# Kernel tuning notes

Measured on AMD Instinct MI355X. Metric: run time of the kernel, lower is better.

The kernel has to match this reference:

```python
import jax, jax.numpy as jnp
import numpy as np

B = 2048      # graphs per side
NPG = 40      # nodes per graph
N = B * NPG   # 81920 total nodes
E = 4 * N     # 327680 directed edges
IN_DIM = 74
H = 256
ADD = 8
GCR_LAYERS = 5
MLP1, MLP2 = 1024, 512


def setup_inputs() -> dict:
    key = jax.random.key(0)
    ks = jax.random.split(key, 24)
    n2g = jnp.repeat(jnp.arange(B, dtype=jnp.int32), NPG)
    s = 0.05
    d = {
        'cat_src': jax.random.randint(ks[0], (E,), 0, N, dtype=jnp.int32),
        'cat_dst': jax.random.randint(ks[1], (E,), 0, N, dtype=jnp.int32),
        'cat_n2g': n2g,
        'cat_x': jax.random.normal(ks[2], (N, IN_DIM), jnp.float32),
        'an_src': jax.random.randint(ks[3], (E,), 0, N, dtype=jnp.int32),
        'an_dst': jax.random.randint(ks[4], (E,), 0, N, dtype=jnp.int32),
        'an_n2g': n2g,
        'an_x': jax.random.normal(ks[5], (N, IN_DIM), jnp.float32),
        'add_features': jax.random.normal(ks[6], (B, ADD), jnp.float32),
        # shared GNN params (same module processes cation and anion)
        'W0': jax.random.normal(ks[7], (IN_DIM, H), jnp.float32) * s,
        'b0': jnp.zeros((H,), jnp.float32),
        'gcrW': jax.random.normal(ks[8], (GCR_LAYERS, 2, H, H), jnp.float32) * s,
        'gcrb': jnp.zeros((GCR_LAYERS, 2, H), jnp.float32),
        # MLP head: (2H + ADD) -> 1024 -> 512 -> 1
        'mW1': jax.random.normal(ks[9], (2 * H + ADD, MLP1), jnp.float32) * s,
        'mb1': jnp.zeros((MLP1,), jnp.float32),
        'mW2': jax.random.normal(ks[10], (MLP1, MLP2), jnp.float32) * s,
        'mb2': jnp.zeros((MLP2,), jnp.float32),
        'mW3': jax.random.normal(ks[11], (MLP2, 1), jnp.float32) * s,
        'mb3': jnp.zeros((1,), jnp.float32),
    }
    return d


def _graph_conv(src, dst, x, W, b):
    # DGL GraphConv, norm='both': out = D_in^{-1/2} A^T D_out^{-1/2} x W + b
    ones = jnp.ones(src.shape[0], x.dtype)
    deg_out = jnp.clip(jax.ops.segment_sum(ones, src, num_segments=N), 1.0)
    deg_in = jnp.clip(jax.ops.segment_sum(ones, dst, num_segments=N), 1.0)
    h = x * jax.lax.rsqrt(deg_out)[:, None]
    agg = jax.ops.segment_sum(h[src], dst, num_segments=N)  # [N, d]
    return (agg * jax.lax.rsqrt(deg_in)[:, None]) @ W + b


def _feat_extract(src, dst, n2g, x, W0, b0, gcrW, gcrb):
    h = _graph_conv(src, dst, x, W0, b0)  # no activation after first conv
    for i in range(GCR_LAYERS):
        o1 = _graph_conv(src, dst, h, gcrW[i, 0], gcrb[i, 0])
        o2 = _graph_conv(src, dst, jax.nn.relu(o1), gcrW[i, 1], gcrb[i, 1])
        h = jax.nn.relu(o2)  # res_connection = 0 -> plain replace
    # dgl.sum_nodes readout per graph
    return jax.ops.segment_sum(h, n2g, num_segments=B)  # [B, H]


def _leaky(x):
    return jnp.where(x > 0, x, 0.01 * x)  # nn.LeakyReLU default slope


def reference(cat_src, cat_dst, cat_n2g, cat_x, an_src, an_dst, an_n2g, an_x,
              add_features, W0, b0, gcrW, gcrb, mW1, mb1, mW2, mb2, mW3, mb3):
    cat_feat = _feat_extract(cat_src, cat_dst, cat_n2g, cat_x, W0, b0, gcrW, gcrb)
    an_feat = _feat_extract(an_src, an_dst, an_n2g, an_x, W0, b0, gcrW, gcrb)
    z = jnp.concatenate([cat_feat, an_feat, add_features], axis=1)  # [B, 2H+ADD]
    h = _leaky(z @ mW1 + mb1)
    h = _leaky(h @ mW2 + mb2)
    out = h @ mW3 + mb3  # [B, 1]
    return out.squeeze(-1)
```

## Files before the change

### kernel.cpp

```cpp
#include <hip/hip_runtime.h>


#define NN 81920
#define NN2 163840
#define NE 327680
#define NE2 655360
#define NB 2048
#define NB2 4096
#define H 256
#define INDIM 74
#define KPAD 128
#define ZK 576
#define DEGCAP 32
#define BSTAGE 24
#define TM 64
#define CPITCH 132

typedef unsigned short u16;
typedef __attribute__((ext_vector_type(8))) short short8;
typedef __attribute__((ext_vector_type(4))) float f32x4;

__device__ inline u16 f2b(float f) {
    unsigned u = __builtin_bit_cast(unsigned, f);
    u += 0x7fffu + ((u >> 16) & 1u);
    return (u16)(u >> 16);
}
__device__ inline float b2f(u16 b) {
    unsigned u = ((unsigned)b) << 16;
    return __builtin_bit_cast(float, u);
}
__device__ inline float blo(unsigned u) { return __builtin_bit_cast(float, u << 16); }
__device__ inline float bhi(unsigned u) { return __builtin_bit_cast(float, u & 0xffff0000u); }

__global__ void fill_kernel(const int* __restrict__ cs, const int* __restrict__ cd,
                            const int* __restrict__ as_, const int* __restrict__ ad,
                            int* __restrict__ dego, int* __restrict__ cnti,
                            int* __restrict__ bucket) {
    int e = blockIdx.x * 256 + threadIdx.x;
    if (e < NE2) {
        int s, d;
        if (e < NE) { s = cs[e]; d = cd[e]; }
        else        { s = as_[e - NE] + NN; d = ad[e - NE] + NN; }
        atomicAdd(&dego[s], 1);
        int p = atomicAdd(&cnti[d], 1);
        if (p < DEGCAP) bucket[(size_t)p * NN2 + d] = s;
    }
}

__global__ void rsqrt_kernel(const int* __restrict__ dego, const int* __restrict__ cnti,
                             float* __restrict__ rso, float* __restrict__ rsi) {
    int i = blockIdx.x * 256 + threadIdx.x;
    if (i < NN2) {
        rso[i] = rsqrtf((float)(dego[i] > 1 ? dego[i] : 1));
        rsi[i] = rsqrtf((float)(cnti[i] > 1 ? cnti[i] : 1));
    }
}

__global__ __launch_bounds__(256) void prescale_x_kernel(
        const float* __restrict__ cx, const float* __restrict__ ax,
        const float* __restrict__ rso, u16* __restrict__ xbp) {
    int t = threadIdx.x;
    int node = blockIdx.x * 4 + (t >> 6);
    int lane = t & 63;
    const float* x = (node < NN) ? (cx + (size_t)node * INDIM)
                                 : (ax + (size_t)(node - NN) * INDIM);
    float w = rso[node];
    int f0 = lane * 2, f1 = f0 + 1;
    u16 a = (f0 < INDIM) ? f2b(x[f0] * w) : (u16)0;
    u16 b = (f1 < INDIM) ? f2b(x[f1] * w) : (u16)0;
    ((unsigned*)xbp)[(size_t)node * 64 + lane] = a | ((unsigned)b << 16);
}

__global__ void prep_w0_kernel(const float* __restrict__ W0, u16* __restrict__ Wt0) {
    int i = blockIdx.x * 256 + threadIdx.x;
    int n = i >> 7, k = i & 127;
    float v = (k < INDIM) ? W0[(size_t)k * H + n] : 0.f;
    Wt0[i] = f2b(v);
}

__global__ void prep_gcr_kernel(const float* __restrict__ W, u16* __restrict__ Wt) {
    int i = blockIdx.x * 256 + threadIdx.x;
    int l = blockIdx.y;
    int n = i >> 8, k = i & 255;
    Wt[(size_t)l * 65536 + i] = f2b(W[(size_t)l * 65536 + (size_t)k * H + n]);
}

__global__ void prep_w1_kernel(const float* __restrict__ W, u16* __restrict__ Wt) {
    int i = blockIdx.x * 256 + threadIdx.x;
    if (i >= 1024 * ZK) return;
    int n = i / ZK, k = i - n * ZK;
    float v = (k < 520) ? W[(size_t)k * 1024 + n] : 0.f;
    Wt[i] = f2b(v);
}

__global__ void prep_w2_kernel(const float* __restrict__ W, u16* __restrict__ Wt) {
    int i = blockIdx.x * 256 + threadIdx.x;
    int n = i >> 10, k = i & 1023;
    Wt[i] = f2b(W[(size_t)k * 512 + n]);
}

__device__ inline void ldg_lds16(const u16* g, u16* l) {
    __builtin_amdgcn_global_load_lds(
        (const __attribute__((address_space(1))) unsigned int*)g,
        (__attribute__((address_space(3))) unsigned int*)l, 16, 0, 0);
}
__device__ inline float actf(float v, int act) {
    if (act == 1) return fmaxf(v, 0.f);
    if (act == 2) return (v > 0.f) ? v : 0.01f * v;
    return v;
}

template <int KD, bool RSO>
__global__ __launch_bounds__(512, 6) void fused_conv_kernel(
        const u16* __restrict__ hIn, const int* __restrict__ bucket,
        const int* __restrict__ cnti, const float* __restrict__ rso,
        const float* __restrict__ rsi, const u16* __restrict__ Bt,
        const float* __restrict__ bias, u16* __restrict__ hOut,
        int act) {
    constexpr int NCH = KD / 8;
    constexpr int KT  = KD / 64;
    __shared__ __align__(16) u16 smem[TM * KD + 8192];
    u16* As = smem;
    u16* Bs = smem + TM * KD;
    int* bkLds = (int*)Bs;
    int* cntL  = (int*)Bs + BSTAGE * TM;

    int t = threadIdx.x;
    int n0 = blockIdx.x * TM;

#pragma unroll
    for (int i = 0; i < (BSTAGE * TM) / 512; ++i) {
        int idx = i * 512 + t;
        bkLds[idx] = bucket[(size_t)(idx >> 6) * NN2 + n0 + (idx & 63)];
    }
    if (t < TM) cntL[t] = cnti[n0 + t];
    __syncthreads();

    for (int i = 0; i < (TM * NCH) / 512; ++i) {
        int gid = i * 512 + t;
        int nl = gid / NCH;
        int ch = gid - nl * NCH;
        int node = n0 + nl;
        int deg = cntL[nl]; if (deg > DEGCAP) deg = DEGCAP;
        int degL = deg < BSTAGE ? deg : BSTAGE;
        const int* bkcol = bkLds + nl;
        int fc = ch * 8;
        int s0 = (deg > 0) ? bkcol[0] : node;
        int sx[8];
#pragma unroll
        for (int s = 0; s < 8; ++s) {
            int raw = bkcol[s * TM];
            sx[s] = (s < degL) ? raw : s0;
        }
        uint4 vx[8];
#pragma unroll
        for (int s = 0; s < 8; ++s)
            vx[s] = *(const uint4*)(hIn + (size_t)sx[s] * KD + fc);
        float wx[8];
#pragma unroll
        for (int s = 0; s < 8; ++s) {
            float rw = RSO ? rso[sx[s]] : 1.f;
            wx[s] = (s < degL) ? rw : 0.f;
        }
        float acc[8] = {};
#pragma unroll
        for (int s = 0; s < 8; ++s) {
            acc[0] += blo(vx[s].x) * wx[s];
            acc[1] += bhi(vx[s].x) * wx[s];
            acc[2] += blo(vx[s].y) * wx[s];
            acc[3] += bhi(vx[s].y) * wx[s];
            acc[4] += blo(vx[s].z) * wx[s];
            acc[5] += bhi(vx[s].z) * wx[s];
            acc[6] += blo(vx[s].w) * wx[s];
            acc[7] += bhi(vx[s].w) * wx[s];
        }
        for (int base = 8; base < degL; base += 4) {
            int i0 = bkcol[(base + 0) * TM];
            int i1 = (base + 1 < degL) ? bkcol[(base + 1) * TM] : i0;
            int i2 = (base + 2 < degL) ? bkcol[(base + 2) * TM] : i0;
            int i3 = (base + 3 < degL) ? bkcol[(base + 3) * TM] : i0;
            float w0 = (RSO ? rso[i0] : 1.f);
            float w1 = (base + 1 < degL) ? (RSO ? rso[i1] : 1.f) : 0.f;
            float w2 = (base + 2 < degL) ? (RSO ? rso[i2] : 1.f) : 0.f;
            float w3 = (base + 3 < degL) ? (RSO ? rso[i3] : 1.f) : 0.f;
            uint4 v0 = *(const uint4*)(hIn + (size_t)i0 * KD + fc);
            uint4 v1 = *(const uint4*)(hIn + (size_t)i1 * KD + fc);
            uint4 v2 = *(const uint4*)(hIn + (size_t)i2 * KD + fc);
            uint4 v3 = *(const uint4*)(hIn + (size_t)i3 * KD + fc);
            acc[0] += blo(v0.x) * w0 + blo(v1.x) * w1 + blo(v2.x) * w2 + blo(v3.x) * w3;
            acc[1] += bhi(v0.x) * w0 + bhi(v1.x) * w1 + bhi(v2.x) * w2 + bhi(v3.x) * w3;
            acc[2] += blo(v0.y) * w0 + blo(v1.y) * w1 + blo(v2.y) * w2 + blo(v3.y) * w3;
            acc[3] += bhi(v0.y) * w0 + bhi(v1.y) * w1 + bhi(v2.y) * w2 + bhi(v3.y) * w3;
            acc[4] += blo(v0.z) * w0 + blo(v1.z) * w1 + blo(v2.z) * w2 + blo(v3.z) * w3;
            acc[5] += bhi(v0.z) * w0 + bhi(v1.z) * w1 + bhi(v2.z) * w2 + bhi(v3.z) * w3;
            acc[6] += blo(v0.w) * w0 + blo(v1.w) * w1 + blo(v2.w) * w2 + blo(v3.w) * w3;
            acc[7] += bhi(v0.w) * w0 + bhi(v1.w) * w1 + bhi(v2.w) * w2 + bhi(v3.w) * w3;
        }
        if (deg > BSTAGE) {
            for (int base = BSTAGE; base < deg; base += 4) {
                int i0 = bucket[(size_t)(base + 0) * NN2 + node];
                int i1 = (base + 1 < deg) ? bucket[(size_t)(base + 1) * NN2 + node] : i0;
                int i2 = (base + 2 < deg) ? bucket[(size_t)(base + 2) * NN2 + node] : i0;
                int i3 = (base + 3 < deg) ? bucket[(size_t)(base + 3) * NN2 + node] : i0;
                float w0 = (RSO ? rso[i0] : 1.f);
                float w1 = (base + 1 < deg) ? (RSO ? rso[i1] : 1.f) : 0.f;
                float w2 = (base + 2 < deg) ? (RSO ? rso[i2] : 1.f) : 0.f;
                float w3 = (base + 3 < deg) ? (RSO ? rso[i3] : 1.f) : 0.f;
                uint4 v0 = *(const uint4*)(hIn + (size_t)i0 * KD + fc);
                uint4 v1 = *(const uint4*)(hIn + (size_t)i1 * KD + fc);
                uint4 v2 = *(const uint4*)(hIn + (size_t)i2 * KD + fc);
                uint4 v3 = *(const uint4*)(hIn + (size_t)i3 * KD + fc);
                acc[0] += blo(v0.x) * w0 + blo(v1.x) * w1 + blo(v2.x) * w2 + blo(v3.x) * w3;
                acc[1] += bhi(v0.x) * w0 + bhi(v1.x) * w1 + bhi(v2.x) * w2 + bhi(v3.x) * w3;
                acc[2] += blo(v0.y) * w0 + blo(v1.y) * w1 + blo(v2.y) * w2 + blo(v3.y) * w3;
                acc[3] += bhi(v0.y) * w0 + bhi(v1.y) * w1 + bhi(v2.y) * w2 + bhi(v3.y) * w3;
                acc[4] += blo(v0.z) * w0 + blo(v1.z) * w1 + blo(v2.z) * w2 + blo(v3.z) * w3;
                acc[5] += bhi(v0.z) * w0 + bhi(v1.z) * w1 + bhi(v2.z) * w2 + bhi(v3.z) * w3;
                acc[6] += blo(v0.w) * w0 + blo(v1.w) * w1 + blo(v2.w) * w2 + blo(v3.w) * w3;
                acc[7] += bhi(v0.w) * w0 + bhi(v1.w) * w1 + bhi(v2.w) * w2 + bhi(v3.w) * w3;
            }
        }
        float ri = rsi[node];
        u16 o[8];
#pragma unroll
        for (int j = 0; j < 8; ++j) o[j] = f2b(acc[j] * ri);
        uint4 ov;
        ov.x = o[0] | ((unsigned)o[1] << 16);
        ov.y = o[2] | ((unsigned)o[3] << 16);
        ov.z = o[4] | ((unsigned)o[5] << 16);
        ov.w = o[6] | ((unsigned)o[7] << 16);
        int kt = ch >> 3, seg = ch & 7;
        *(uint4*)(As + (size_t)kt * (TM * 64) + nl * 64 + ((seg ^ (nl & 7)) * 8)) = ov;
    }
    __syncthreads();

    int wave = t >> 6, lane = t & 63;
    int wr = wave >> 2, wc = wave & 3;
    int mrow = lane & 15, q = lane >> 4;

    f32x4 acc[2][4] = {};
    for (int kt = 0; kt < KT; ++kt) {
        const u16* Ak = As + kt * (TM * 64);
#pragma unroll
        for (int nh = 0; nh < 2; ++nh) {
#pragma unroll
            for (int c = 0; c < 2; ++c) {
                int cidx = c * 512 + t;
                int row = cidx >> 3, seg = cidx & 7;
                int ks = ((seg ^ (row & 7))) * 8;
                ldg_lds16(Bt + (size_t)(nh * 128 + row) * KD + kt * 64 + ks,
                          Bs + (size_t)(c * 512 + wave * 64) * 8);
            }
            __syncthreads();
#pragma unroll
            for (int kk = 0; kk < 2; ++kk) {
                short8 a[2], b[2];
#pragma unroll
                for (int mt = 0; mt < 2; ++mt) {
                    int row = wr * 32 + mt * 16 + mrow;
                    int seg = (kk * 4 + q) ^ (row & 7);
                    a[mt] = *(const short8*)(Ak + row * 64 + seg * 8);
                }
#pragma unroll
                for (int nt = 0; nt < 2; ++nt) {
                    int row = wc * 32 + nt * 16 + mrow;
                    int seg = (kk * 4 + q) ^ (row & 7);
                    b[nt] = *(const short8*)(Bs + row * 64 + seg * 8);
                }
#pragma unroll
                for (int mt = 0; mt < 2; ++mt)
#pragma unroll
                    for (int nt = 0; nt < 2; ++nt)
                        acc[mt][nh * 2 + nt] = __builtin_amdgcn_mfma_f32_16x16x32_bf16(
                            a[mt], b[nt], acc[mt][nh * 2 + nt], 0, 0, 0);
            }
            __syncthreads();
        }
    }

#pragma unroll
    for (int nh = 0; nh < 2; ++nh) {
#pragma unroll
        for (int mt = 0; mt < 2; ++mt) {
            int rl = wr * 32 + mt * 16 + q * 4;
#pragma unroll
            for (int nt = 0; nt < 2; ++nt) {
                int cl = wc * 32 + nt * 16 + mrow;
                float bv = bias[nh * 128 + cl];
#pragma unroll
                for (int qq = 0; qq < 4; ++qq) {
                    float v = actf(acc[mt][nh * 2 + nt][qq] + bv, act);
                    smem[(size_t)(rl + qq) * CPITCH + cl] = f2b(v);
                }
            }
        }
        __syncthreads();
        int rr = t >> 4, sg = t & 15;
#pragma unroll
        for (int pass = 0; pass < 2; ++pass) {
            int row = pass * 32 + rr;
            uint4 val = *(const uint4*)(smem + (size_t)row * CPITCH + sg * 8);
            *(uint4*)(hOut + (size_t)(n0 + row) * 256 + nh * 128 + sg * 8) = val;
        }
        __syncthreads();
    }
}

__global__ __launch_bounds__(256) void gemm_mfma_kernel(
        const u16* __restrict__ A, int lda,
        const u16* __restrict__ Bt, int ldb,
        const float* __restrict__ bias, u16* __restrict__ C, int ldc,
        int Kiters, int act) {
    __shared__ __align__(16) u16 smem[128 * CPITCH];
    u16* As = smem;
    u16* Bs = smem + 8192;
    int t = threadIdx.x;
    int wave = t >> 6, lane = t & 63;
    int wr = wave >> 1, wc = wave & 1;
    int row0 = blockIdx.y * 128, col0 = blockIdx.x * 128;

    int sr = t >> 3;
    int ksrc = (((t & 7) ^ (sr & 7))) * 8;
    const u16* Ag[4];
    const u16* Bg[4];
#pragma unroll
    for (int c = 0; c < 4; ++c) {
        Ag[c] = A + (size_t)(row0 + c * 32 + sr) * lda + ksrc;
        Bg[c] = Bt + (size_t)(col0 + c * 32 + sr) * ldb + ksrc;
    }
    u16* AsW = As + wave * 512;
    u16* BsW = Bs + wave * 512;

    f32x4 acc[4][4] = {};
    int mrow = lane & 15;
    int q = lane >> 4;

    for (int kt = 0; kt < Kiters; ++kt) {
#pragma unroll
        for (int c = 0; c < 4; ++c) ldg_lds16(Ag[c], AsW + c * 2048);
#pragma unroll
        for (int c = 0; c < 4; ++c) ldg_lds16(Bg[c], BsW + c * 2048);
        __syncthreads();
#pragma unroll
        for (int kk = 0; kk < 2; ++kk) {
            short8 a[4], b[4];
#pragma unroll
            for (int mt = 0; mt < 4; ++mt) {
                int row = wr * 64 + mt * 16 + mrow;
                int seg = (kk * 4 + q) ^ (row & 7);
                a[mt] = *(const short8*)(As + row * 64 + seg * 8);
            }
#pragma unroll
            for (int nt = 0; nt < 4; ++nt) {
                int row = wc * 64 + nt * 16 + mrow;
                int seg = (kk * 4 + q) ^ (row & 7);
                b[nt] = *(const short8*)(Bs + row * 64 + seg * 8);
            }
#pragma unroll
            for (int mt = 0; mt < 4; ++mt)
#pragma unroll
                for (int nt = 0; nt < 4; ++nt)
                    acc[mt][nt] = __builtin_amdgcn_mfma_f32_16x16x32_bf16(
                        a[mt], b[nt], acc[mt][nt], 0, 0, 0);
        }
        __syncthreads();
#pragma unroll
        for (int c = 0; c < 4; ++c) { Ag[c] += 64; Bg[c] += 64; }
    }

#pragma unroll
    for (int mt = 0; mt < 4; ++mt) {
        int rl = wr * 64 + mt * 16 + q * 4;
#pragma unroll
        for (int nt = 0; nt < 4; ++nt) {
            int cl = wc * 64 + nt * 16 + mrow;
            float bv = bias[col0 + cl];
#pragma unroll
            for (int qq = 0; qq < 4; ++qq) {
                float v = actf(acc[mt][nt][qq] + bv, act);
                smem[(size_t)(rl + qq) * CPITCH + cl] = f2b(v);
            }
        }
    }
    __syncthreads();
    int rr = t >> 4;
    int seg = t & 15;
#pragma unroll
    for (int pass = 0; pass < 8; ++pass) {
        int row = pass * 16 + rr;
        uint4 val = *(const uint4*)(smem + (size_t)row * CPITCH + seg * 8);
        *(uint4*)(C + (size_t)(row0 + row) * ldc + col0 + seg * 8) = val;
    }
}

__global__ __launch_bounds__(256) void pool_kernel(const u16* __restrict__ h,
                                                   u16* __restrict__ z) {
    int g = blockIdx.x, f = threadIdx.x;
    float acc = 0.f;
    const u16* base = h + (size_t)g * 40 * H + f;
#pragma unroll
    for (int j = 0; j < 40; ++j) acc += b2f(base[j * H]);
    int zrow = g & (NB - 1);
    int zoff = (g >> 11) * H;
    z[(size_t)zrow * ZK + zoff + f] = f2b(acc);
}

__global__ void copy_add_kernel(const float* __restrict__ add, u16* __restrict__ z) {
    int i = blockIdx.x * 256 + threadIdx.x;
    if (i < NB * 8) {
        int g = i >> 3, a = i & 7;
        z[(size_t)g * ZK + 512 + a] = f2b(add[i]);
    }
}

__global__ void gemv_out_kernel(const u16* __restrict__ A, const float* __restrict__ w,
                                const float* __restrict__ b, float* __restrict__ out, int K) {
    int wave = threadIdx.x >> 6;
    int lane = threadIdx.x & 63;
    int row = blockIdx.x * 4 + wave;
    float acc = 0.f;
    for (int k = lane; k < K; k += 64) acc += b2f(A[(size_t)row * K + k]) * w[k];
#pragma unroll
    for (int off = 32; off > 0; off >>= 1) acc += __shfl_down(acc, off, 64);
    if (lane == 0) out[row] = acc + b[0];
}

extern "C" void kernel_launch(void* const* d_in, const int* in_sizes, int n_in,
                              void* d_out, int out_size, void* d_ws, size_t ws_size,
                              hipStream_t stream) {
    const int*   cat_src = (const int*)d_in[0];
    const int*   cat_dst = (const int*)d_in[1];
    const float* cat_x   = (const float*)d_in[3];
    const int*   an_src  = (const int*)d_in[4];
    const int*   an_dst  = (const int*)d_in[5];
    const float* an_x    = (const float*)d_in[7];
    const float* add_f   = (const float*)d_in[8];
    const float* W0      = (const float*)d_in[9];
    const float* b0      = (const float*)d_in[10];
    const float* gcrW    = (const float*)d_in[11];
    const float* gcrb    = (const float*)d_in[12];
    const float* mW1     = (const float*)d_in[13];
    const float* mb1     = (const float*)d_in[14];
    const float* mW2     = (const float*)d_in[15];
    const float* mb2     = (const float*)d_in[16];
    const float* mW3     = (const float*)d_in[17];
    const float* mb3     = (const float*)d_in[18];
    float* out = (float*)d_out;

    char* p = (char*)d_ws;
    auto alloc = [&](size_t bytes) -> void* {
        void* rp = (void*)p;
        p += (bytes + 255) & ~(size_t)255;
        return rp;
    };
    int*   dego   = (int*)alloc((size_t)NN2 * 4);
    int*   cnti   = (int*)alloc((size_t)NN2 * 4);
    int*   bucket = (int*)alloc((size_t)NN2 * DEGCAP * 4);
    float* rso    = (float*)alloc((size_t)NN2 * 4);
    float* rsi    = (float*)alloc((size_t)NN2 * 4);
    u16*   hA     = (u16*)alloc((size_t)NN2 * H * 2);
    u16*   hB     = (u16*)alloc((size_t)NN2 * H * 2);
    u16*   Wt0    = (u16*)alloc((size_t)H * KPAD * 2);
    u16*   Wtg    = (u16*)alloc((size_t)10 * H * H * 2);
    u16*   Wt1    = (u16*)alloc((size_t)1024 * ZK * 2);
    u16*   Wt2    = (u16*)alloc((size_t)512 * 1024 * 2);
    u16*   zb     = (u16*)alloc((size_t)NB * ZK * 2);
    u16*   m1b    = (u16*)alloc((size_t)NB * 1024 * 2);
    u16*   m2b    = (u16*)alloc((size_t)NB * 512 * 2);
    u16*   xbp    = hA;
    (void)ws_size; (void)in_sizes; (void)n_in; (void)out_size;

    prep_w0_kernel<<<(H * KPAD) / 256, 256, 0, stream>>>(W0, Wt0);
    prep_gcr_kernel<<<dim3(H * H / 256, 10), 256, 0, stream>>>(gcrW, Wtg);
    prep_w1_kernel<<<(1024 * ZK + 255) / 256, 256, 0, stream>>>(mW1, Wt1);
    prep_w2_kernel<<<(512 * 1024) / 256, 256, 0, stream>>>(mW2, Wt2);
    hipMemsetAsync(zb, 0, (size_t)NB * ZK * 2, stream);
    hipMemsetAsync(dego, 0, (size_t)NN2 * 4, stream);
    hipMemsetAsync(cnti, 0, (size_t)NN2 * 4, stream);

    fill_kernel<<<NE2 / 256, 256, 0, stream>>>(cat_src, cat_dst, an_src, an_dst,
                                               dego, cnti, bucket);
    rsqrt_kernel<<<NN2 / 256, 256, 0, stream>>>(dego, cnti, rso, rsi);

    prescale_x_kernel<<<NN2 / 4, 256, 0, stream>>>(cat_x, an_x, rso, xbp);
    fused_conv_kernel<KPAD, false><<<NN2 / TM, 512, 0, stream>>>(
        xbp, bucket, cnti, rso, rsi, Wt0, b0, hB, 0);

    for (int l = 0; l < 10; ++l) {
        const u16* hin = (l & 1) ? hA : hB;
        u16*       hout = (l & 1) ? hB : hA;
        fused_conv_kernel<H, true><<<NN2 / TM, 512, 0, stream>>>(
            hin, bucket, cnti, rso, rsi, Wtg + (size_t)l * H * H,
            gcrb + (size_t)l * H, hout, 1);
    }
    pool_kernel<<<NB2, 256, 0, stream>>>(hB, zb);
    copy_add_kernel<<<(NB * 8 + 255) / 256, 256, 0, stream>>>(add_f, zb);

    gemm_mfma_kernel<<<dim3(1024 / 128, NB / 128), 256, 0, stream>>>(
        zb, ZK, Wt1, ZK, mb1, m1b, 1024, ZK / 64, 2);
    gemm_mfma_kernel<<<dim3(512 / 128, NB / 128), 256, 0, stream>>>(
        m1b, 1024, Wt2, 1024, mb2, m2b, 512, 1024 / 64, 2);
    gemv_out_kernel<<<NB / 4, 256, 0, stream>>>(m2b, mW3, mb3, out, 512);
}
```

Baseline: 1.237 ms.

## Halve fused conv node tile to 32 rows and stage all bucket slots in LDS

```diff
diff --git a/kernel.cpp b/kernel.cpp
--- a/kernel.cpp
+++ b/kernel.cpp
@@ -12,8 +12,8 @@
 #define KPAD 128
 #define ZK 576
 #define DEGCAP 32
-#define BSTAGE 24
-#define TM 64
+#define BSTAGE 32
+#define TM 32
 #define CPITCH 132
 
 typedef unsigned short u16;
@@ -111,7 +111,7 @@
 }
 
 template <int KD, bool RSO>
-__global__ __launch_bounds__(512, 6) void fused_conv_kernel(
+__global__ __launch_bounds__(512, 8) void fused_conv_kernel(
         const u16* __restrict__ hIn, const int* __restrict__ bucket,
         const int* __restrict__ cnti, const float* __restrict__ rso,
         const float* __restrict__ rsi, const u16* __restrict__ Bt,
@@ -131,7 +131,7 @@
 #pragma unroll
     for (int i = 0; i < (BSTAGE * TM) / 512; ++i) {
         int idx = i * 512 + t;
-        bkLds[idx] = bucket[(size_t)(idx >> 6) * NN2 + n0 + (idx & 63)];
+        bkLds[idx] = bucket[(size_t)(idx >> 5) * NN2 + n0 + (idx & 31)];
     }
     if (t < TM) cntL[t] = cnti[n0 + t];
     __syncthreads();
@@ -142,7 +142,6 @@
         int ch = gid - nl * NCH;
         int node = n0 + nl;
         int deg = cntL[nl]; if (deg > DEGCAP) deg = DEGCAP;
-        int degL = deg < BSTAGE ? deg : BSTAGE;
         const int* bkcol = bkLds + nl;
         int fc = ch * 8;
         int s0 = (deg > 0) ? bkcol[0] : node;
@@ -150,7 +149,7 @@
 #pragma unroll
         for (int s = 0; s < 8; ++s) {
             int raw = bkcol[s * TM];
-            sx[s] = (s < degL) ? raw : s0;
+            sx[s] = (s < deg) ? raw : s0;
         }
         uint4 vx[8];
 #pragma unroll
@@ -160,7 +159,7 @@
 #pragma unroll
         for (int s = 0; s < 8; ++s) {
             float rw = RSO ? rso[sx[s]] : 1.f;
-            wx[s] = (s < degL) ? rw : 0.f;
+            wx[s] = (s < deg) ? rw : 0.f;
         }
         float acc[8] = {};
 #pragma unroll
@@ -174,15 +173,15 @@
             acc[6] += blo(vx[s].w) * wx[s];
             acc[7] += bhi(vx[s].w) * wx[s];
         }
-        for (int base = 8; base < degL; base += 4) {
+        for (int base = 8; base < deg; base += 4) {
             int i0 = bkcol[(base + 0) * TM];
-            int i1 = (base + 1 < degL) ? bkcol[(base + 1) * TM] : i0;
-            int i2 = (base + 2 < degL) ? bkcol[(base + 2) * TM] : i0;
-            int i3 = (base + 3 < degL) ? bkcol[(base + 3) * TM] : i0;
+            int i1 = (base + 1 < deg) ? bkcol[(base + 1) * TM] : i0;
+            int i2 = (base + 2 < deg) ? bkcol[(base + 2) * TM] : i0;
+            int i3 = (base + 3 < deg) ? bkcol[(base + 3) * TM] : i0;
             float w0 = (RSO ? rso[i0] : 1.f);
-            float w1 = (base + 1 < degL) ? (RSO ? rso[i1] : 1.f) : 0.f;
-            float w2 = (base + 2 < degL) ? (RSO ? rso[i2] : 1.f) : 0.f;
-            float w3 = (base + 3 < degL) ? (RSO ? rso[i3] : 1.f) : 0.f;
+            float w1 = (base + 1 < deg) ? (RSO ? rso[i1] : 1.f) : 0.f;
+            float w2 = (base + 2 < deg) ? (RSO ? rso[i2] : 1.f) : 0.f;
+            float w3 = (base + 3 < deg) ? (RSO ? rso[i3] : 1.f) : 0.f;
             uint4 v0 = *(const uint4*)(hIn + (size_t)i0 * KD + fc);
             uint4 v1 = *(const uint4*)(hIn + (size_t)i1 * KD + fc);
             uint4 v2 = *(const uint4*)(hIn + (size_t)i2 * KD + fc);
@@ -196,30 +195,6 @@
             acc[6] += blo(v0.w) * w0 + blo(v1.w) * w1 + blo(v2.w) * w2 + blo(v3.w) * w3;
             acc[7] += bhi(v0.w) * w0 + bhi(v1.w) * w1 + bhi(v2.w) * w2 + bhi(v3.w) * w3;
         }
-        if (deg > BSTAGE) {
-            for (int base = BSTAGE; base < deg; base += 4) {
-                int i0 = bucket[(size_t)(base + 0) * NN2 + node];
-                int i1 = (base + 1 < deg) ? bucket[(size_t)(base + 1) * NN2 + node] : i0;
-                int i2 = (base + 2 < deg) ? bucket[(size_t)(base + 2) * NN2 + node] : i0;
-                int i3 = (base + 3 < deg) ? bucket[(size_t)(base + 3) * NN2 + node] : i0;
-                float w0 = (RSO ? rso[i0] : 1.f);
-                float w1 = (base + 1 < deg) ? (RSO ? rso[i1] : 1.f) : 0.f;
-                float w2 = (base + 2 < deg) ? (RSO ? rso[i2] : 1.f) : 0.f;
-                float w3 = (base + 3 < deg) ? (RSO ? rso[i3] : 1.f) : 0.f;
-                uint4 v0 = *(const uint4*)(hIn + (size_t)i0 * KD + fc);
-                uint4 v1 = *(const uint4*)(hIn + (size_t)i1 * KD + fc);
-                uint4 v2 = *(const uint4*)(hIn + (size_t)i2 * KD + fc);
-                uint4 v3 = *(const uint4*)(hIn + (size_t)i3 * KD + fc);
-                acc[0] += blo(v0.x) * w0 + blo(v1.x) * w1 + blo(v2.x) * w2 + blo(v3.x) * w3;
-                acc[1] += bhi(v0.x) * w0 + bhi(v1.x) * w1 + bhi(v2.x) * w2 + bhi(v3.x) * w3;
-                acc[2] += blo(v0.y) * w0 + blo(v1.y) * w1 + blo(v2.y) * w2 + blo(v3.y) * w3;
-                acc[3] += bhi(v0.y) * w0 + bhi(v1.y) * w1 + bhi(v2.y) * w2 + bhi(v3.y) * w3;
-                acc[4] += blo(v0.z) * w0 + blo(v1.z) * w1 + blo(v2.z) * w2 + blo(v3.z) * w3;
-                acc[5] += bhi(v0.z) * w0 + bhi(v1.z) * w1 + bhi(v2.z) * w2 + bhi(v3.z) * w3;
-                acc[6] += blo(v0.w) * w0 + blo(v1.w) * w1 + blo(v2.w) * w2 + blo(v3.w) * w3;
-                acc[7] += bhi(v0.w) * w0 + bhi(v1.w) * w1 + bhi(v2.w) * w2 + bhi(v3.w) * w3;
-            }
-        }
         float ri = rsi[node];
         u16 o[8];
 #pragma unroll
@@ -238,7 +213,7 @@
     int wr = wave >> 2, wc = wave & 3;
     int mrow = lane & 15, q = lane >> 4;
 
-    f32x4 acc[2][4] = {};
+    f32x4 acc[4] = {};
     for (int kt = 0; kt < KT; ++kt) {
         const u16* Ak = As + kt * (TM * 64);
 #pragma unroll
@@ -254,12 +229,11 @@
             __syncthreads();
 #pragma unroll
             for (int kk = 0; kk < 2; ++kk) {
-                short8 a[2], b[2];
-#pragma unroll
-                for (int mt = 0; mt < 2; ++mt) {
-                    int row = wr * 32 + mt * 16 + mrow;
+                short8 a0, b[2];
+                {
+                    int row = wr * 16 + mrow;
                     int seg = (kk * 4 + q) ^ (row & 7);
-                    a[mt] = *(const short8*)(Ak + row * 64 + seg * 8);
+                    a0 = *(const short8*)(Ak + row * 64 + seg * 8);
                 }
 #pragma unroll
                 for (int nt = 0; nt < 2; ++nt) {
@@ -268,11 +242,9 @@
                     b[nt] = *(const short8*)(Bs + row * 64 + seg * 8);
                 }
 #pragma unroll
-                for (int mt = 0; mt < 2; ++mt)
-#pragma unroll
-                    for (int nt = 0; nt < 2; ++nt)
-                        acc[mt][nh * 2 + nt] = __builtin_amdgcn_mfma_f32_16x16x32_bf16(
-                            a[mt], b[nt], acc[mt][nh * 2 + nt], 0, 0, 0);
+                for (int nt = 0; nt < 2; ++nt)
+                    acc[nh * 2 + nt] = __builtin_amdgcn_mfma_f32_16x16x32_bf16(
+                        a0, b[nt], acc[nh * 2 + nt], 0, 0, 0);
             }
             __syncthreads();
         }
@@ -280,28 +252,23 @@
 
 #pragma unroll
     for (int nh = 0; nh < 2; ++nh) {
-#pragma unroll
-        for (int mt = 0; mt < 2; ++mt) {
-            int rl = wr * 32 + mt * 16 + q * 4;
+        {
+            int rl = wr * 16 + q * 4;
 #pragma unroll
             for (int nt = 0; nt < 2; ++nt) {
                 int cl = wc * 32 + nt * 16 + mrow;
                 float bv = bias[nh * 128 + cl];
 #pragma unroll
                 for (int qq = 0; qq < 4; ++qq) {
-                    float v = actf(acc[mt][nh * 2 + nt][qq] + bv, act);
+                    float v = actf(acc[nh * 2 + nt][qq] + bv, act);
                     smem[(size_t)(rl + qq) * CPITCH + cl] = f2b(v);
                 }
             }
         }
         __syncthreads();
         int rr = t >> 4, sg = t & 15;
-#pragma unroll
-        for (int pass = 0; pass < 2; ++pass) {
-            int row = pass * 32 + rr;
-            uint4 val = *(const uint4*)(smem + (size_t)row * CPITCH + sg * 8);
-            *(uint4*)(hOut + (size_t)(n0 + row) * 256 + nh * 128 + sg * 8) = val;
-        }
+        uint4 val = *(const uint4*)(smem + (size_t)rr * CPITCH + sg * 8);
+        *(uint4*)(hOut + (size_t)(n0 + rr) * 256 + nh * 128 + sg * 8) = val;
         __syncthreads();
     }
 }
```

Measured after the change: 1.395 ms. 1.13x slower.
